# Kernel optimization log

Measured on AMD Instinct MI355X. Metric: run time of the kernel, lower is better.

The kernel has to match this reference:

```python
import jax, jax.numpy as jnp
import numpy as np

N = 8192
INPUT_DIM = 256
HIDDEN_DIM = 16
K_NEIGHBORS = 6


def setup_inputs() -> dict:
    key = jax.random.key(0)
    k1, k2 = jax.random.split(key)
    x = jax.random.normal(k1, (N, INPUT_DIM), dtype=jnp.float32)
    W = jax.random.normal(k2, (HIDDEN_DIM, INPUT_DIM), dtype=jnp.float32) * (1.0 / np.sqrt(INPUT_DIM))
    b = jnp.zeros((HIDDEN_DIM,), dtype=jnp.float32)
    return {"x": x, "W": W, "b": b}


def reference(x, W, b):
    num_nodes = x.shape[0]
    # Linear projection then L2-normalize rows (F.normalize, p=2, dim=1, eps=1e-12)
    h = x @ W.T + b                                   # [N, H]
    norm = jnp.linalg.norm(h, axis=1, keepdims=True)
    h = h / jnp.maximum(norm, 1e-12)
    sim = h @ h.T                                     # [N, N] cosine similarity
    k = min(K_NEIGHBORS, num_nodes - 1)
    # top-(k+1) per row; drop the first (self, sim=1 is the max)
    top_vals, top_idx = jax.lax.top_k(sim, k + 1)     # [N, k+1]
    neigh_idx = top_idx[:, 1:]                        # [N, k]
    neigh_vals = top_vals[:, 1:]                      # [N, k]
    rows = jnp.arange(num_nodes)[:, None]             # [N, 1]
    adj = jnp.zeros_like(sim).at[rows, neigh_idx].set(neigh_vals)
    adj = (adj + adj.T) * 0.5
    row_sums = adj.sum(axis=1, keepdims=True)
    adj = adj / (row_sums + 1e-8)
    return adj
```

## Files before the change

kernel.cpp:

```cpp
#include <hip/hip_runtime.h>
#include <stdint.h>
#include <math.h>

#define NN   8192
#define IND  256
#define HID  16
#define KN   6
#define SEG  8
#define SW   (NN/SEG)
#define CCOL 256
#define NCH  (SW/CCOL)
#define TPC  (CCOL/16)
#define ZPB  16384

typedef short s8v  __attribute__((ext_vector_type(8)));
typedef float f4v  __attribute__((ext_vector_type(4)));

__device__ __forceinline__ uint32_t bf16_rne_bits(float x) {
    const uint32_t u = __float_as_uint(x);
    return (u + 0x7FFFu + ((u >> 16) & 1u)) & 0xFFFF0000u;
}

#define CSWPD(X,i,j) { const double _h = fmax(X[i], X[j]); const double _l = fmin(X[i], X[j]); X[i] = _h; X[j] = _l; }
#define CSWPS(a,b)   { const double _h = fmax(a, b); const double _l = fmin(a, b); a = _h; b = _l; }
#define BSTAGESD(X) CSWPD(X,0,4) CSWPD(X,1,5) CSWPD(X,2,6) CSWPD(X,3,7) \
                    CSWPD(X,0,2) CSWPD(X,1,3) CSWPD(X,4,6) CSWPD(X,5,7) \
                    CSWPD(X,0,1) CSWPD(X,2,3) CSWPD(X,4,5) CSWPD(X,6,7)

__device__ __forceinline__ void bar_nodrain() {
    __builtin_amdgcn_sched_barrier(0);
    __builtin_amdgcn_s_barrier();
    __builtin_amdgcn_sched_barrier(0);
}
__device__ __forceinline__ void wait_lgkm0() {
    asm volatile("s_waitcnt lgkmcnt(0)" ::: "memory");
    __builtin_amdgcn_sched_barrier(0);
}

__global__ __launch_bounds__(256) void k1_embed(const float* __restrict__ x,
                                                const float* __restrict__ W,
                                                const float* __restrict__ b,
                                                float* __restrict__ rs,
                                                ushort* __restrict__ PA1,
                                                ushort* __restrict__ PA2,
                                                ushort* __restrict__ PA3,
                                                ushort* __restrict__ PB1,
                                                ushort* __restrict__ PB2)
{
    __shared__ float sh[4][16];
    const int lane = threadIdx.x & 63;
    const int wv   = threadIdx.x >> 6;
    const int row  = blockIdx.x * 4 + wv;

    const float4 xv = *(const float4*)(x + (size_t)row * IND + lane * 4);

    float acc[HID];
#pragma unroll
    for (int k = 0; k < HID; ++k) {
        const float4 wv4 = *(const float4*)(W + (size_t)k * IND + lane * 4);
        float v = xv.x * wv4.x + xv.y * wv4.y + xv.z * wv4.z + xv.w * wv4.w;
#pragma unroll
        for (int m = 32; m >= 1; m >>= 1) v += __shfl_xor(v, m, 64);
        acc[k] = v;
    }

    if (lane == 0) {
        float hv[HID];
        float ss = 0.f;
#pragma unroll
        for (int k = 0; k < HID; ++k) { hv[k] = acc[k] + b[k]; ss += hv[k] * hv[k]; }
        const float nrm = fmaxf(sqrtf(ss), 1e-12f);
#pragma unroll
        for (int k = 0; k < HID; ++k) sh[wv][k] = hv[k] / nrm;
        rs[row] = 0.f;
    }
    __syncthreads();

    if (lane < 32) {
        const int s = lane;
        const int k = s & 15;
        const float xval = sh[wv][k];
        const uint32_t hb = bf16_rne_bits(xval);
        const float r1 = xval - __uint_as_float(hb);
        const uint32_t mb = bf16_rne_bits(r1);
        const float r2 = r1 - __uint_as_float(mb);
        const uint32_t lb = bf16_rne_bits(r2);
        const ushort hi = (ushort)(hb >> 16);
        const ushort mi = (ushort)(mb >> 16);
        const ushort lo = (ushort)(lb >> 16);
        const bool f = (s < 16);
        const size_t t = (size_t)row * 32 + s;
        PA1[t] = hi;
        PA2[t] = f ? mi : hi;
        PA3[t] = f ? lo : mi;
        PB1[t] = f ? hi : mi;
        PB2[t] = f ? hi : lo;
    }
}

__global__ __launch_bounds__(256, 4) void p1_scan(const ushort* __restrict__ PA1,
                                                  const ushort* __restrict__ PA2,
                                                  const ushort* __restrict__ PA3,
                                                  const ushort* __restrict__ PB1,
                                                  const ushort* __restrict__ PB2,
                                                  double* __restrict__ tqd,
                                                  f4v* __restrict__ outz)
{
    __shared__ s8v lds[2048];

    const int tid  = threadIdx.x;
    const int lane = tid & 63;
    const int wv   = tid >> 6;
    const int seg  = blockIdx.x & (SEG - 1);
    const int row0 = (blockIdx.x >> 3) * 64 + wv * 16;
    const int n    = lane & 15;
    const int q    = lane >> 4;
    const int qs   = (q + ((n >> 1) & 3)) & 3;

    const size_t ioff = ((size_t)(row0 + n) << 5) + (q << 3);
    const s8v i1 = *(const s8v*)(PA1 + ioff);
    const s8v i2 = *(const s8v*)(PA2 + ioff);
    const s8v i3 = *(const s8v*)(PA3 + ioff);

    const f4v zf = {0.f, 0.f, 0.f, 0.f};

    double L[8];
#pragma unroll
    for (int t = 0; t < 8; ++t) L[t] = 0.0;

    for (int cc = 0; cc < NCH; ++cc) {
        bar_nodrain();

        s8v sv[8];
#pragma unroll
        for (int it = 0; it < 8; ++it) {
            const int o  = it * 256 + tid;
            const int oo = o & 1023;
            const int c  = oo >> 2;
            const int qq = oo & 3;
            const ushort* src = (it < 4) ? PB1 : PB2;
            const int gcol = seg * SW + cc * CCOL + c;
            sv[it] = *(const s8v*)(src + ((size_t)gcol << 5) + (qq << 3));
        }
        __builtin_amdgcn_sched_barrier(0);

        {
            const size_t zb = (size_t)blockIdx.x * ZPB + (size_t)cc * 4096 + tid;
#pragma unroll
            for (int z = 0; z < 16; ++z)
                __builtin_nontemporal_store(zf, outz + zb + z * 256);
        }
        __builtin_amdgcn_sched_barrier(0);

#pragma unroll
        for (int it = 0; it < 8; ++it) {
            const int o  = it * 256 + tid;
            const int oo = o & 1023;
            const int c  = oo >> 2;
            const int qq = oo & 3;
            const int sw = (qq + ((c >> 1) & 3)) & 3;
            lds[((it < 4) ? 0 : 1024) + (c << 2) + sw] = sv[it];
        }
        wait_lgkm0();
        bar_nodrain();

        const int base = (n << 2) + qs;
        const int a0   = seg * SW + cc * CCOL + (q << 2);
#pragma unroll 2
        for (int t = 0; t < TPC; ++t) {
            const s8v jb1 = lds[t * 64 + base];
            const s8v jb2 = lds[1024 + t * 64 + base];

            f4v acc = {0.f, 0.f, 0.f, 0.f};
            acc = __builtin_amdgcn_mfma_f32_16x16x32_bf16(jb1, i1, acc, 0, 0, 0);
            acc = __builtin_amdgcn_mfma_f32_16x16x32_bf16(jb2, i2, acc, 0, 0, 0);
            acc = __builtin_amdgcn_mfma_f32_16x16x32_bf16(jb1, i3, acc, 0, 0, 0);

            const int tb = 8191 - (a0 + (t << 4));
            double kd[4];
#pragma unroll
            for (int g = 0; g < 4; ++g) {
                kd[g] = __longlong_as_double(
                    __double_as_longlong((double)acc[g] + 2.0) |
                    (long long)(unsigned)(tb - g));
            }

            double s0 = kd[0], s1 = kd[1], s2 = kd[2], s3 = kd[3];
            CSWPS(s0, s1) CSWPS(s2, s3) CSWPS(s0, s2) CSWPS(s1, s3) CSWPS(s1, s2)

            L[4] = fmax(L[4], s3);
            L[5] = fmax(L[5], s2);
            L[6] = fmax(L[6], s1);
            L[7] = fmax(L[7], s0);
            BSTAGESD(L)
        }
    }

#pragma unroll
    for (int mm = 16; mm <= 32; mm <<= 1) {
        double o[8], X[8];
#pragma unroll
        for (int t = 0; t < 8; ++t) o[t] = __shfl_xor(L[t], mm, 64);
#pragma unroll
        for (int t = 0; t < 8; ++t) X[t] = fmax(L[t], o[7 - t]);
        BSTAGESD(X)
#pragma unroll
        for (int t = 0; t < 8; ++t) L[t] = X[t];
    }

    if (q == 0) {
        double* dst = tqd + ((size_t)seg * NN + (row0 + n)) * 8;
#pragma unroll
        for (int t = 0; t < 8; ++t) dst[t] = L[t];
    }
}

__global__ __launch_bounds__(256) void p2_merge(const double* __restrict__ tqd,
                                                float* __restrict__ rs,
                                                int* __restrict__ ni,
                                                float* __restrict__ nv)
{
    const int lane = threadIdx.x & 63;
    const int wv   = threadIdx.x >> 6;
    const int row  = blockIdx.x * 4 + wv;
    const int s    = lane >> 3;
    const int t    = lane & 7;

    double key = tqd[((size_t)s * NN + row) * 8 + t];
    float sum = 0.f;

#pragma unroll
    for (int r = 0; r < 7; ++r) {
        double m = key;
#pragma unroll
        for (int mm = 1; mm < 64; mm <<= 1) {
            const double o = __shfl_xor(m, mm, 64);
            m = fmax(m, o);
        }
        const long long mb = __double_as_longlong(m);
        if (r >= 1) {
            const float v  = (float)(__longlong_as_double(mb & ~0x1FFFLL) - 2.0);
            const int tie  = (int)(mb & 0x1FFFLL);
            const int j    = NN - 1 - tie;
            sum += v;
            if (__double_as_longlong(key) == mb) {
                nv[(size_t)row * KN + (r - 1)] = v;
                ni[(size_t)row * KN + (r - 1)] = j;
                atomicAdd(&rs[j], 0.5f * v);
            }
        }
        if (__double_as_longlong(key) == mb)
            key = 0.0;
    }

    if (lane == 0) atomicAdd(&rs[row], 0.5f * sum);
}

__global__ __launch_bounds__(256) void k5_scatter(const int* __restrict__ nbr_idx,
                                                  const float* __restrict__ nbr_val,
                                                  const float* __restrict__ rs,
                                                  float* __restrict__ out)
{
    const int e = blockIdx.x * 256 + threadIdx.x;
    const int i = e / KN;
    const int j = nbr_idx[e];
    const float v = nbr_val[e] * 0.5f;
    const float wi = v / (rs[i] + 1e-8f);
    const float wj = v / (rs[j] + 1e-8f);
    atomicAdd(out + (size_t)i * NN + j, wi);
    atomicAdd(out + (size_t)j * NN + i, wj);
}

extern "C" void kernel_launch(void* const* d_in, const int* in_sizes, int n_in,
                              void* d_out, int out_size, void* d_ws, size_t ws_size,
                              hipStream_t stream)
{
    const float* x = (const float*)d_in[0];
    const float* W = (const float*)d_in[1];
    const float* b = (const float*)d_in[2];
    float* out = (float*)d_out;

    double* tqd  = (double*)d_ws;
    float*  rs   = (float*)(tqd + (size_t)SEG * NN * 8);
    float*  nv   = rs + NN;
    int*    ni   = (int*)(nv + (size_t)NN * KN);
    ushort* PA1  = (ushort*)(ni + (size_t)NN * KN);
    ushort* PA2  = PA1 + (size_t)NN * 32;
    ushort* PA3  = PA2 + (size_t)NN * 32;
    ushort* PB1  = PA3 + (size_t)NN * 32;
    ushort* PB2  = PB1 + (size_t)NN * 32;

    k1_embed <<<NN / 4,           256, 0, stream>>>(x, W, b, rs, PA1, PA2, PA3, PB1, PB2);
    p1_scan  <<<(NN / 64) * SEG,  256, 0, stream>>>(PA1, PA2, PA3, PB1, PB2, tqd, (f4v*)out);
    p2_merge <<<NN / 4,           256, 0, stream>>>(tqd, rs, ni, nv);
    k5_scatter<<<(NN * KN) / 256, 256, 0, stream>>>(ni, nv, rs, out);
}
```

Before: 324.4 us.

## Merge two MFMA tiles per top-k merge step and move zero stores after barrier

The inner loop now computes two 16-column tiles per iteration, sorts their 8 candidate keys into a full bitonic sequence, and merges all 8 into the running top-8 list in one bitonic merge. This replaces one sort-4 plus merge per tile, roughly halving the merge work on the running list. The global loads now go straight into LDS without a register staging array, and the nontemporal zero stores to the output move after the barrier so they overlap with compute. The cost is more registers per iteration and possibly less overlap of the global load latency.

```diff
diff --git a/kernel.cpp b/kernel.cpp
--- a/kernel.cpp
+++ b/kernel.cpp
@@ -22,7 +22,6 @@
 }
 
 #define CSWPD(X,i,j) { const double _h = fmax(X[i], X[j]); const double _l = fmin(X[i], X[j]); X[i] = _h; X[j] = _l; }
-#define CSWPS(a,b)   { const double _h = fmax(a, b); const double _l = fmin(a, b); a = _h; b = _l; }
 #define BSTAGESD(X) CSWPD(X,0,4) CSWPD(X,1,5) CSWPD(X,2,6) CSWPD(X,3,7) \
                     CSWPD(X,0,2) CSWPD(X,1,3) CSWPD(X,4,6) CSWPD(X,5,7) \
                     CSWPD(X,0,1) CSWPD(X,2,3) CSWPD(X,4,5) CSWPD(X,6,7)
@@ -131,27 +130,6 @@
     for (int cc = 0; cc < NCH; ++cc) {
         bar_nodrain();
 
-        s8v sv[8];
-#pragma unroll
-        for (int it = 0; it < 8; ++it) {
-            const int o  = it * 256 + tid;
-            const int oo = o & 1023;
-            const int c  = oo >> 2;
-            const int qq = oo & 3;
-            const ushort* src = (it < 4) ? PB1 : PB2;
-            const int gcol = seg * SW + cc * CCOL + c;
-            sv[it] = *(const s8v*)(src + ((size_t)gcol << 5) + (qq << 3));
-        }
-        __builtin_amdgcn_sched_barrier(0);
-
-        {
-            const size_t zb = (size_t)blockIdx.x * ZPB + (size_t)cc * 4096 + tid;
-#pragma unroll
-            for (int z = 0; z < 16; ++z)
-                __builtin_nontemporal_store(zf, outz + zb + z * 256);
-        }
-        __builtin_amdgcn_sched_barrier(0);
-
 #pragma unroll
         for (int it = 0; it < 8; ++it) {
             const int o  = it * 256 + tid;
@@ -159,39 +137,61 @@
             const int c  = oo >> 2;
             const int qq = oo & 3;
             const int sw = (qq + ((c >> 1) & 3)) & 3;
-            lds[((it < 4) ? 0 : 1024) + (c << 2) + sw] = sv[it];
-        }
+            const ushort* src = (it < 4) ? PB1 : PB2;
+            const int gcol = seg * SW + cc * CCOL + c;
+            const s8v v = *(const s8v*)(src + ((size_t)gcol << 5) + (qq << 3));
+            lds[((it < 4) ? 0 : 1024) + (c << 2) + sw] = v;
+        }
+
         wait_lgkm0();
         bar_nodrain();
+
+        {
+            const size_t zb = (size_t)blockIdx.x * ZPB + (size_t)cc * 4096 + tid;
+#pragma unroll
+            for (int z = 0; z < 16; ++z)
+                __builtin_nontemporal_store(zf, outz + zb + z * 256);
+        }
 
         const int base = (n << 2) + qs;
         const int a0   = seg * SW + cc * CCOL + (q << 2);
 #pragma unroll 2
-        for (int t = 0; t < TPC; ++t) {
-            const s8v jb1 = lds[t * 64 + base];
-            const s8v jb2 = lds[1024 + t * 64 + base];
-
-            f4v acc = {0.f, 0.f, 0.f, 0.f};
-            acc = __builtin_amdgcn_mfma_f32_16x16x32_bf16(jb1, i1, acc, 0, 0, 0);
-            acc = __builtin_amdgcn_mfma_f32_16x16x32_bf16(jb2, i2, acc, 0, 0, 0);
-            acc = __builtin_amdgcn_mfma_f32_16x16x32_bf16(jb1, i3, acc, 0, 0, 0);
-
-            const int tb = 8191 - (a0 + (t << 4));
-            double kd[4];
+        for (int t = 0; t < TPC; t += 2) {
+            const s8v jb1a = lds[t * 64 + base];
+            const s8v jb2a = lds[1024 + t * 64 + base];
+            const s8v jb1b = lds[(t + 1) * 64 + base];
+            const s8v jb2b = lds[1024 + (t + 1) * 64 + base];
+
+            f4v accA = {0.f, 0.f, 0.f, 0.f};
+            accA = __builtin_amdgcn_mfma_f32_16x16x32_bf16(jb1a, i1, accA, 0, 0, 0);
+            accA = __builtin_amdgcn_mfma_f32_16x16x32_bf16(jb2a, i2, accA, 0, 0, 0);
+            accA = __builtin_amdgcn_mfma_f32_16x16x32_bf16(jb1a, i3, accA, 0, 0, 0);
+
+            f4v accB = {0.f, 0.f, 0.f, 0.f};
+            accB = __builtin_amdgcn_mfma_f32_16x16x32_bf16(jb1b, i1, accB, 0, 0, 0);
+            accB = __builtin_amdgcn_mfma_f32_16x16x32_bf16(jb2b, i2, accB, 0, 0, 0);
+            accB = __builtin_amdgcn_mfma_f32_16x16x32_bf16(jb1b, i3, accB, 0, 0, 0);
+
+            const int tbA = 8191 - (a0 + (t << 4));
+            const int tbB = tbA - 16;
+            double X[8];
 #pragma unroll
             for (int g = 0; g < 4; ++g) {
-                kd[g] = __longlong_as_double(
-                    __double_as_longlong((double)acc[g] + 2.0) |
-                    (long long)(unsigned)(tb - g));
+                X[g] = __longlong_as_double(
+                    __double_as_longlong((double)accA[g] + 2.0) |
+                    (long long)(unsigned)(tbA - g));
+                X[7 - g] = __longlong_as_double(
+                    __double_as_longlong((double)accB[g] + 2.0) |
+                    (long long)(unsigned)(tbB - g));
             }
 
-            double s0 = kd[0], s1 = kd[1], s2 = kd[2], s3 = kd[3];
-            CSWPS(s0, s1) CSWPS(s2, s3) CSWPS(s0, s2) CSWPS(s1, s3) CSWPS(s1, s2)
-
-            L[4] = fmax(L[4], s3);
-            L[5] = fmax(L[5], s2);
-            L[6] = fmax(L[6], s1);
-            L[7] = fmax(L[7], s0);
+            CSWPD(X, 0, 1) CSWPD(X, 2, 3) CSWPD(X, 0, 2) CSWPD(X, 1, 3) CSWPD(X, 1, 2)
+            CSWPD(X, 7, 6) CSWPD(X, 5, 4) CSWPD(X, 7, 5) CSWPD(X, 6, 4) CSWPD(X, 6, 5)
+
+            BSTAGESD(X)
+
+#pragma unroll
+            for (int i = 0; i < 8; ++i) L[i] = fmax(L[i], X[7 - i]);
             BSTAGESD(L)
         }
     }
```

New measurement: 322.5 us. No clear change (-0.6%).
